# Kernel optimization log

Hardware: AMD Instinct MI355X
Metric: run time of the kernel (lower is better)

The kernel has to match this reference:

```python
import jax, jax.numpy as jnp
import numpy as np
from jax import lax

DT = 1.0 / 120.0
B, T = 4096, 128
TWO_PI = 2.0 * np.pi


def setup_inputs() -> dict:
    key = jax.random.key(0)
    k1, k2, k3, k4 = jax.random.split(key, 4)
    return {
        "params": jax.random.normal(k1, (4,), jnp.float32),
        "covariance_params": jax.random.normal(k2, (7,), jnp.float32),
        "init_states": jax.random.normal(k3, (B, 6), jnp.float32),
        "measurements": jax.random.normal(k4, (B, T, 3), jnp.float32),
    }


def _wrap(a):
    # wrap angle innovation to [-pi, pi]
    return a - TWO_PI * jnp.round(a / TWO_PI)


def _smooth_loss(params, covariance_params, init_state, z):
    # z: [T, 3] measurements of (x, y, theta)
    friction = (jnp.tanh(params[0]) + 1.0) * 0.01
    damping = (jnp.tanh(params[1]) + 1.0) * 0.01
    cp = jax.nn.sigmoid(covariance_params)
    R = jnp.diag(cp[:3])                                    # [3,3] meas noise
    Q = jnp.diag(cp[jnp.array([3, 3, 4, 4, 5, 6])])         # [6,6] proc noise
    I6 = jnp.eye(6, dtype=z.dtype)
    Hm = jnp.zeros((3, 6), z.dtype).at[0, 0].set(1.).at[1, 1].set(1.).at[2, 4].set(1.)
    P0 = 0.01 * I6

    def f_and_F(s):
        # free-sliding puck dynamics: [x, y, dx, dy, th, dth]
        x, y, dx, dy, th, dth = s
        ndx = dx - DT * (damping * dx + friction * jnp.tanh(100. * dx))
        ndy = dy - DT * (damping * dy + friction * jnp.tanh(100. * dy))
        ndth = dth * (1.0 - DT * damping)
        ns = jnp.stack([x + DT * dx, y + DT * dy, ndx, ndy, th + DT * dth, ndth])
        gx = 1.0 - DT * (damping + friction * 100. * (1. - jnp.tanh(100. * dx) ** 2))
        gy = 1.0 - DT * (damping + friction * 100. * (1. - jnp.tanh(100. * dy) ** 2))
        F = (I6.at[0, 2].set(DT).at[1, 3].set(DT).at[4, 5].set(DT)
               .at[2, 2].set(gx).at[3, 3].set(gy).at[5, 5].set(1.0 - DT * damping))
        return ns, F

    def ekf_step(carry, zt):
        s, P = carry
        sp, F = f_and_F(s)
        Pp = F @ P @ F.T + Q
        S = Hm @ Pp @ Hm.T + R
        innov = zt - Hm @ sp
        innov = innov.at[2].set(_wrap(innov[2]))
        K = jnp.linalg.solve(S, Hm @ Pp).T          # Pp H^T S^-1
        s_new = sp + K @ innov
        P_new = (I6 - K @ Hm) @ Pp
        return (s_new, P_new), (s_new, P_new, sp, Pp, F)

    _, (sf, Pf, sp, Pp, Fs) = lax.scan(ekf_step, (init_state, P0), z)

    # RTS backward pass
    def rts_step(carry, inp):
        s_next, P_next = carry
        s_f, P_f, sp_n, Pp_n, F_n = inp
        G = jnp.linalg.solve(Pp_n, F_n @ P_f).T     # P_f F^T Pp^{-1}
        s_s = s_f + G @ (s_next - sp_n)
        P_s = P_f + G @ (P_next - Pp_n) @ G.T
        return (s_s, P_s), (s_s, P_s)

    inp = (sf[:-1], Pf[:-1], sp[1:], Pp[1:], Fs[1:])
    _, (s_sm_head, P_sm_head) = lax.scan(rts_step, (sf[-1], Pf[-1]), inp, reverse=True)
    s_sm = jnp.concatenate([s_sm_head, sf[-1:]], 0)   # [T,6]
    P_sm = jnp.concatenate([P_sm_head, Pf[-1:]], 0)   # [T,6,6]

    # log-lik style loss vs measurements[2:] (as in compute_loss)
    zz, st, Pt = z[2:], s_sm[2:], P_sm[2:]
    Sv = jnp.einsum('ij,tjk,lk->til', Hm, Pt, Hm) + R  # [T-2,3,3] meas-space var
    innov_xy = zz[:, :2] - st[:, :2]
    a = zz[:, 2] - st[:, 4]
    a = jnp.where(a > 1.5 * np.pi, a - TWO_PI, a)
    a = jnp.where(a < -1.5 * np.pi, a + TWO_PI, a)
    innov = jnp.concatenate([innov_xy, a[:, None]], 1)
    sign, logdet = jnp.linalg.slogdet(Sv)
    return jnp.sum(sign * jnp.exp(logdet) + jnp.einsum('ti,tij,tj->t', innov, Sv, innov))


def reference(params, covariance_params, init_states, measurements):
    per_seg = jax.vmap(_smooth_loss, in_axes=(None, None, 0, 0))(
        params, covariance_params, init_states, measurements)
    return jnp.sum(per_seg)
```

## Files before the change

### kernel.cpp

```cpp
#include <hip/hip_runtime.h>
#include <cmath>


namespace {

constexpr int B = 4096;
constexpr int T = 128;
constexpr int NT = B * 3;
constexpr int CPB = 64;
constexpr int NBLK = NT / CPB;
constexpr int RBLK = 256;
constexpr int RTH = 256;

constexpr float DTc     = 1.0f / 120.0f;
constexpr float TWO_PIc = 6.28318530717958647692f;
constexpr float PI_1_5  = 4.71238898038468985769f;
constexpr float INV_2PI = 0.15915494309189533577f;

__device__ __forceinline__ float frcp(float x) { return __builtin_amdgcn_rcpf(x); }

__device__ __forceinline__ float fast_tanh(float x) {
  float e = __expf(2.0f * x);
  return 1.0f - 2.0f * frcp(e + 1.0f);
}
__device__ __forceinline__ float sigmoidf(float x) {
  return frcp(1.0f + __expf(-x));
}

__global__ __launch_bounds__(CPB, 1) void filt_kernel(
    const float* __restrict__ params, const float* __restrict__ covp,
    const float* __restrict__ init_states, const float* __restrict__ z,
    float* __restrict__ hist1, float2* __restrict__ aq) {
  const int lane = threadIdx.x;
  const int blk  = blockIdx.x;
  const int f    = blk >> 6;
  const int seq  = ((blk & 63) << 6) + lane;
  const int gid  = blk * CPB + lane;

  __shared__ float4 h4s[T * CPB];

  const float friction = (fast_tanh(params[0]) + 1.0f) * 0.01f;
  const float damping  = (fast_tanh(params[1]) + 1.0f) * 0.01f;
  float cp[7];
#pragma unroll
  for (int i = 0; i < 7; i++) cp[i] = sigmoidf(covp[i]);
  const float dcoef = 1.0f - DTc * damping;
  const bool isTH = (f == 2);
  const float q0 = isTH ? cp[5] : cp[3];
  const float q1 = isTH ? cp[6] : cp[4];
  const float r  = cp[f];

  const int pidx = (f == 0) ? 0 : (f == 1) ? 1 : 4;
  const int vidx = (f == 0) ? 2 : (f == 1) ? 3 : 5;
  float p = init_states[seq * 6 + pidx];
  float v = init_states[seq * 6 + vidx];
  float P00 = 0.01f, P01 = 0.0f, P11 = 0.01f;

  const float* __restrict__ zp = z + (size_t)seq * (T * 3) + f;

#pragma unroll 8
  for (int t = 0; t < T; t++) {
    const float zc = zp[t * 3];

    float g, tv;
    if (!isTH) {
      const float th = fast_tanh(100.0f * v);
      tv = v - DTc * (damping * v + friction * th);
      g = 1.0f - DTc * (damping + 100.0f * friction * (1.0f - th * th));
    } else {
      tv = dcoef * v;
      g = dcoef;
    }
    const float tp = p + DTc * v;
    const float u = P01 + DTc * P11;
    const float Pp00 = P00 + DTc * P01 + DTc * u + q0;
    const float Pp01 = g * u;
    const float Pp11 = g * (g * P11) + q1;
    const float iS = frcp(Pp00 + r);
    const float K0 = Pp00 * iS;
    const float K1 = Pp01 * iS;
    float e = zc - tp;
    if (isTH) e = e - TWO_PIc * rintf(e * INV_2PI);
    p = tp + K0 * e;
    v = tv + K1 * e;
    const float om = 1.0f - K0;
    P00 = om * Pp00;
    P01 = om * Pp01;
    P11 = Pp11 - K1 * Pp01;

    h4s[t * CPB + lane] = make_float4(p, v, P00, P01);
    hist1[(size_t)t * NT + gid] = P11;
  }

  {
    float e = zp[(T - 1) * 3] - p;
    if (isTH) {
      if (e >  PI_1_5) e -= TWO_PIc;
      if (e < -PI_1_5) e += TWO_PIc;
    }
    const float a = P00 + r;
    aq[((size_t)f * T + (T - 1)) * B + seq] = make_float2(a, a * e * e);
  }

  float sp_ = p, sv_ = v, Ps00 = P00, Ps01 = P01, Ps11 = P11;

  float h1b[8];
#pragma unroll
  for (int i = 0; i < 8; i++) h1b[i] = hist1[(size_t)(126 - i) * NT + gid];

#pragma unroll 8
  for (int i = 0; i < 128; i++) {
    const int n = 126 - i;
    const int nc = (n < 2) ? 2 : n;
    const int sl = i & 7;
    const float4 h4 = h4s[nc * CPB + lane];
    const float f11 = h1b[sl];
    const int nf = (n >= 10) ? (n - 8) : 2;
    h1b[sl] = hist1[(size_t)nf * NT + gid];
    const float zn_ = zp[nc * 3];

    const float fp = h4.x, fv = h4.y, f00 = h4.z, f01 = h4.w;

    float g, tv;
    if (!isTH) {
      const float th = fast_tanh(100.0f * fv);
      tv = fv - DTc * (damping * fv + friction * th);
      g = 1.0f - DTc * (damping + 100.0f * friction * (1.0f - th * th));
    } else {
      tv = dcoef * fv;
      g = dcoef;
    }
    const float tp = fp + DTc * fv;
    const float u = f01 + DTc * f11;
    const float Pp00 = f00 + DTc * f01 + DTc * u + q0;
    const float Pp01 = g * u;
    const float Pp11 = g * (g * f11) + q1;

    const float idet = frcp(Pp00 * Pp11 - Pp01 * Pp01);
    const float W00 = f00, W01 = DTc * f00 + g * f01;
    const float W10 = f01, W11 = DTc * f01 + g * f11;
    const float G00 = (W00 * Pp11 - W01 * Pp01) * idet;
    const float G01 = (W01 * Pp00 - W00 * Pp01) * idet;
    const float G10 = (W10 * Pp11 - W11 * Pp01) * idet;
    const float G11 = (W11 * Pp00 - W10 * Pp01) * idet;

    const float ds0 = sp_ - tp, ds1 = sv_ - tv;
    const float np = fp + G00 * ds0 + G01 * ds1;
    const float nv = fv + G10 * ds0 + G11 * ds1;

    const float M00 = Ps00 - Pp00, M01 = Ps01 - Pp01, M11 = Ps11 - Pp11;
    const float GM00 = G00 * M00 + G01 * M01, GM01 = G00 * M01 + G01 * M11;
    const float GM10 = G10 * M00 + G11 * M01, GM11 = G10 * M01 + G11 * M11;
    Ps00 = f00 + GM00 * G00 + GM01 * G01;
    Ps01 = f01 + GM00 * G10 + GM01 * G11;
    Ps11 = f11 + GM10 * G10 + GM11 * G11;
    sp_ = np;
    sv_ = nv;

    if (n >= 2) {
      const float a = Ps00 + r;
      float e = zn_ - np;
      if (isTH) {
        if (e >  PI_1_5) e -= TWO_PIc;
        if (e < -PI_1_5) e += TWO_PIc;
      }
      aq[((size_t)f * T + n) * B + seq] = make_float2(a, a * e * e);
    }
  }
}

__global__ __launch_bounds__(RTH) void reduce_kernel(
    const float2* __restrict__ aq, float* __restrict__ out) {
  const int tid = threadIdx.x;
  constexpr int NTERM = 126 * B;
  float part = 0.0f;
  for (int idx = blockIdx.x * RTH + tid; idx < NTERM; idx += RTH * RBLK) {
    const int t = 2 + (idx >> 12);
    const int s = idx & (B - 1);
    const float2 a0 = aq[((size_t)0 * T + t) * B + s];
    const float2 a1 = aq[((size_t)1 * T + t) * B + s];
    const float2 a2 = aq[((size_t)2 * T + t) * B + s];
    part += a0.x * a1.x * a2.x + (a0.y + a1.y + a2.y);
  }
#pragma unroll
  for (int off = 32; off > 0; off >>= 1) part += __shfl_down(part, off);
  __shared__ float red[RTH / 64];
  if ((tid & 63) == 0) red[tid >> 6] = part;
  __syncthreads();
  if (tid == 0) {
    float s = 0.0f;
#pragma unroll
    for (int w = 0; w < RTH / 64; w++) s += red[w];
    atomicAdd(out, s);
  }
}

}

extern "C" void kernel_launch(void* const* d_in, const int* in_sizes, int n_in,
                              void* d_out, int out_size, void* d_ws, size_t ws_size,
                              hipStream_t stream) {
  const float* params      = (const float*)d_in[0];
  const float* covp        = (const float*)d_in[1];
  const float* init_states = (const float*)d_in[2];
  const float* z           = (const float*)d_in[3];
  float* out = (float*)d_out;

  const size_t hist1B = (size_t)T * NT * sizeof(float);
  const size_t aqB    = (size_t)T * NT * sizeof(float2);
  const size_t needBytes = hist1B + aqB;

  hipMemsetAsync(d_out, 0, sizeof(float), stream);

  if (ws_size >= needBytes) {
    float*  hist1 = (float*)d_ws;
    float2* aqp   = (float2*)((char*)d_ws + hist1B);
    filt_kernel<<<NBLK, CPB, 0, stream>>>(params, covp, init_states, z,
                                          hist1, aqp);
    reduce_kernel<<<RBLK, RTH, 0, stream>>>(aqp, out);
  }
}
```

Measured before the change: 134.5 us.

## Transpose measurements into coalesced layout and keep P11 history in LDS

Adds a transpose kernel that rewrites z into a feature-major [3][T][B] layout so the filter kernel reads it with coalesced, register-prefetched loads instead of strided per-sequence reads. The P11 history is moved from a global workspace buffer into shared memory, and the backward pass prefetches LDS entries two steps ahead. This removes the global P11 write/read round trip and the uncoalesced z reads, at the cost of an extra kernel launch, a full pass over z, and more LDS per block, which may limit occupancy.

Result: faster. 124.2 us (-7.7%).

```diff
diff --git a/kernel.cpp b/kernel.cpp
--- a/kernel.cpp
+++ b/kernel.cpp
@@ -27,17 +27,49 @@
   return frcp(1.0f + __expf(-x));
 }
 
+__global__ __launch_bounds__(256) void ztrans_kernel(
+    const float* __restrict__ z, float* __restrict__ zt) {
+  __shared__ float tile[96 * 65];
+  const int tid = threadIdx.x;
+  const int bs = blockIdx.x & 63;
+  const int bt = blockIdx.x >> 6;
+  const int s0 = bs * 64, t0 = bt * 32;
+
+  const float* __restrict__ zbase = z + (size_t)s0 * 384 + t0 * 3;
+#pragma unroll
+  for (int k = 0; k < 6; k++) {
+    const int idx = tid + k * 256;
+    const int sl = idx / 24;
+    const int c4 = idx - sl * 24;
+    const float4 v4 = *(const float4*)(zbase + (size_t)sl * 384 + c4 * 4);
+    tile[(c4 * 4 + 0) * 65 + sl] = v4.x;
+    tile[(c4 * 4 + 1) * 65 + sl] = v4.y;
+    tile[(c4 * 4 + 2) * 65 + sl] = v4.z;
+    tile[(c4 * 4 + 3) * 65 + sl] = v4.w;
+  }
+  __syncthreads();
+#pragma unroll
+  for (int k = 0; k < 24; k++) {
+    const int idx = tid + k * 256;
+    const int r  = idx >> 6;
+    const int sl = idx & 63;
+    const int fc = r >> 5;
+    const int tl = r & 31;
+    zt[((size_t)fc * T + t0 + tl) * B + s0 + sl] = tile[(tl * 3 + fc) * 65 + sl];
+  }
+}
+
 __global__ __launch_bounds__(CPB, 1) void filt_kernel(
     const float* __restrict__ params, const float* __restrict__ covp,
-    const float* __restrict__ init_states, const float* __restrict__ z,
-    float* __restrict__ hist1, float2* __restrict__ aq) {
+    const float* __restrict__ init_states, const float* __restrict__ zt,
+    float2* __restrict__ aq) {
   const int lane = threadIdx.x;
   const int blk  = blockIdx.x;
   const int f    = blk >> 6;
   const int seq  = ((blk & 63) << 6) + lane;
-  const int gid  = blk * CPB + lane;
-
-  __shared__ float4 h4s[T * CPB];
+
+  __shared__ float4 h4s[127 * CPB];
+  __shared__ float  p11s[T * CPB];
 
   const float friction = (fast_tanh(params[0]) + 1.0f) * 0.01f;
   const float damping  = (fast_tanh(params[1]) + 1.0f) * 0.01f;
@@ -56,11 +88,17 @@
   float v = init_states[seq * 6 + vidx];
   float P00 = 0.01f, P01 = 0.0f, P11 = 0.01f;
 
-  const float* __restrict__ zp = z + (size_t)seq * (T * 3) + f;
+  const float* __restrict__ ztf = zt + (size_t)f * T * B + seq;
+
+  float zr[8];
+#pragma unroll
+  for (int k = 0; k < 8; k++) zr[k] = ztf[(size_t)k * B];
 
 #pragma unroll 8
   for (int t = 0; t < T; t++) {
-    const float zc = zp[t * 3];
+    const float zc = zr[t & 7];
+    const int tf = (t < T - 8) ? t + 8 : T - 1;
+    zr[t & 7] = ztf[(size_t)tf * B];
 
     float g, tv;
     if (!isTH) {
@@ -88,12 +126,12 @@
     P01 = om * Pp01;
     P11 = Pp11 - K1 * Pp01;
 
-    h4s[t * CPB + lane] = make_float4(p, v, P00, P01);
-    hist1[(size_t)t * NT + gid] = P11;
+    if (t < 127) h4s[t * CPB + lane] = make_float4(p, v, P00, P01);
+    p11s[t * CPB + lane] = P11;
   }
 
   {
-    float e = zp[(T - 1) * 3] - p;
+    float e = ztf[(size_t)(T - 1) * B] - p;
     if (isTH) {
       if (e >  PI_1_5) e -= TWO_PIc;
       if (e < -PI_1_5) e += TWO_PIc;
@@ -104,20 +142,29 @@
 
   float sp_ = p, sv_ = v, Ps00 = P00, Ps01 = P01, Ps11 = P11;
 
-  float h1b[8];
-#pragma unroll
-  for (int i = 0; i < 8; i++) h1b[i] = hist1[(size_t)(126 - i) * NT + gid];
+  float4 h4r[2];
+  float  p11r[2];
+  float  zrb[8];
+  h4r[0]  = h4s[126 * CPB + lane];
+  p11r[0] = p11s[126 * CPB + lane];
+  h4r[1]  = h4s[125 * CPB + lane];
+  p11r[1] = p11s[125 * CPB + lane];
+#pragma unroll
+  for (int k = 0; k < 8; k++) zrb[k] = ztf[(size_t)(126 - k) * B];
 
 #pragma unroll 8
   for (int i = 0; i < 128; i++) {
     const int n = 126 - i;
-    const int nc = (n < 2) ? 2 : n;
-    const int sl = i & 7;
-    const float4 h4 = h4s[nc * CPB + lane];
-    const float f11 = h1b[sl];
-    const int nf = (n >= 10) ? (n - 8) : 2;
-    h1b[sl] = hist1[(size_t)nf * NT + gid];
-    const float zn_ = zp[nc * 3];
+    const int s2 = i & 1;
+    const int s8 = i & 7;
+    const float4 h4 = h4r[s2];
+    const float f11 = p11r[s2];
+    const float zn_ = zrb[s8];
+    const int nl = (n >= 4) ? n - 2 : 2;
+    h4r[s2]  = h4s[nl * CPB + lane];
+    p11r[s2] = p11s[nl * CPB + lane];
+    const int nz = (n >= 10) ? n - 8 : 2;
+    zrb[s8] = ztf[(size_t)nz * B];
 
     const float fp = h4.x, fv = h4.y, f00 = h4.z, f01 = h4.w;
 
@@ -206,17 +253,17 @@
   const float* z           = (const float*)d_in[3];
   float* out = (float*)d_out;
 
-  const size_t hist1B = (size_t)T * NT * sizeof(float);
-  const size_t aqB    = (size_t)T * NT * sizeof(float2);
-  const size_t needBytes = hist1B + aqB;
+  const size_t ztB = (size_t)T * NT * sizeof(float);
+  const size_t aqB = (size_t)T * NT * sizeof(float2);
+  const size_t needBytes = ztB + aqB;
 
   hipMemsetAsync(d_out, 0, sizeof(float), stream);
 
   if (ws_size >= needBytes) {
-    float*  hist1 = (float*)d_ws;
-    float2* aqp   = (float2*)((char*)d_ws + hist1B);
-    filt_kernel<<<NBLK, CPB, 0, stream>>>(params, covp, init_states, z,
-                                          hist1, aqp);
+    float*  ztp = (float*)d_ws;
+    float2* aqp = (float2*)((char*)d_ws + ztB);
+    ztrans_kernel<<<256, 256, 0, stream>>>(z, ztp);
+    filt_kernel<<<NBLK, CPB, 0, stream>>>(params, covp, init_states, ztp, aqp);
     reduce_kernel<<<RBLK, RTH, 0, stream>>>(aqp, out);
   }
 }
```
